# Kernel optimization log

Measured on AMD Instinct MI355X. Metric: run time of the kernel, lower is better.

The kernel has to match this reference:

```python
import jax, jax.numpy as jnp
import numpy as np

B, QS, KS = 8, 1024, 1024
QDIM = KDIM = VDIM = 512
HEADS, ODIM = 8, 64
NEG_SLOPE = 0.2


def setup_inputs() -> dict:
    key = jax.random.key(0)
    ks = jax.random.split(key, 7)
    return {
        "Q": jax.random.normal(ks[0], (B, QS, QDIM), jnp.float32),
        "K": jax.random.normal(ks[1], (B, KS, KDIM), jnp.float32),
        "V": jax.random.normal(ks[2], (B, KS, VDIM), jnp.float32),
        # torch Linear weights: (out_features, in_features)
        "WQ": jax.random.normal(ks[3], (HEADS, QDIM), jnp.float32) * 0.05,
        "WK": jax.random.normal(ks[4], (HEADS, KDIM), jnp.float32) * 0.05,
        "WV": jax.random.normal(ks[5], (HEADS * ODIM, VDIM), jnp.float32) * 0.05,
        "bias": jax.random.normal(ks[6], (HEADS, ODIM), jnp.float32) * 0.05,
    }


def reference(Q, K, V, WQ, WK, WV, bias):
    b, qs = Q.shape[:2]
    Vproj = (V @ WV.T).reshape(b, -1, HEADS, ODIM)          # (b, k, h, d)
    attn_K = K @ WK.T                                        # (b, k, h)
    attn_Q = Q @ WQ.T                                        # (b, q, h)
    # additive GAT-style scores: (b, q, k, h)
    w = jax.nn.leaky_relu(attn_Q[:, :, None, :] + attn_K[:, None, :, :],
                          negative_slope=NEG_SLOPE)
    w = jax.nn.softmax(w, axis=2)                            # softmax over keys
    out = jnp.einsum('bqkh,bkhd->bqhd', w, Vproj) + bias     # (b, q, h, d)
    return out.reshape(b, qs, -1)
```

## Files before the change

### kernel.cpp

```cpp
#include <hip/hip_runtime.h>
#include <hip/hip_bf16.h>

#define NS 0.2f


typedef _Float16 half8 __attribute__((ext_vector_type(8)));
typedef float f32x4 __attribute__((ext_vector_type(4)));

__global__ __launch_bounds__(256) void stage1_kernel(
    const float* __restrict__ Q, const float* __restrict__ K,
    const float* __restrict__ V, const float* __restrict__ WQ,
    const float* __restrict__ WK, const float* __restrict__ WV,
    float* __restrict__ aQ, float* __restrict__ aK,
    _Float16* __restrict__ Vp) {
  __shared__ __align__(16) float smem[4096];
  int bid = blockIdx.x;
  int t = threadIdx.x;
  if (bid < 4096) {
    const float* X;
    const float* W;
    float* aX;
    int rb;
    if (bid < 2048) { X = Q; W = WQ; aX = aQ; rb = bid; }
    else            { X = K; W = WK; aX = aK; rb = bid - 2048; }
    float* Wl = smem;
#pragma unroll
    for (int i = 0; i < 16; i++) Wl[i * 256 + t] = W[i * 256 + t];
    __syncthreads();
    int w = t >> 6, lane = t & 63;
    int row = rb * 4 + w;
    const float* x = X + (size_t)row * 512;
    float4 x0 = *(const float4*)(x + lane * 4);
    float4 x1 = *(const float4*)(x + 256 + lane * 4);
    float acc[8];
#pragma unroll
    for (int h = 0; h < 8; h++) {
      const float* wl = Wl + h * 512;
      float4 w0 = *(const float4*)(wl + lane * 4);
      float4 w1 = *(const float4*)(wl + 256 + lane * 4);
      float a = x0.x * w0.x + x0.y * w0.y + x0.z * w0.z + x0.w * w0.w +
                x1.x * w1.x + x1.y * w1.y + x1.z * w1.z + x1.w * w1.w;
#pragma unroll
      for (int off = 32; off > 0; off >>= 1) a += __shfl_xor(a, off);
      acc[h] = a;
    }
    if (lane == 0) {
      float* o = aX + (size_t)row * 8;
      o[0] = acc[0]; o[1] = acc[1]; o[2] = acc[2]; o[3] = acc[3];
      o[4] = acc[4]; o[5] = acc[5]; o[6] = acc[6]; o[7] = acc[7];
    }
  } else {
    int v = bid - 4096;
    int m0 = (v >> 3) * 64, n0 = (v & 7) * 64;
    _Float16* As = (_Float16*)smem;
    _Float16* Bs = (_Float16*)(smem + 1024);
    int lane = t & 63, wid = t >> 6;
    int wr = wid >> 1, wc = wid & 1;
    int sr = t >> 2, sc = t & 3;
    const float* ap = V + (size_t)(m0 + sr) * 512 + sc * 8;
    const float* bp = WV + (size_t)(n0 + sr) * 512 + sc * 8;
    _Float16* aw = As + sr * 32 + ((sc ^ ((sr >> 1) & 3)) * 8);
    _Float16* bw = Bs + sr * 32 + ((sc ^ ((sr >> 1) & 3)) * 8);
    int fr = lane & 15, fs = lane >> 4;
    f32x4 acc[2][2];
#pragma unroll
    for (int i = 0; i < 2; i++)
#pragma unroll
      for (int j = 0; j < 2; j++)
#pragma unroll
        for (int r = 0; r < 4; r++) acc[i][j][r] = 0.f;

    float4 av0 = *(const float4*)(ap);
    float4 av1 = *(const float4*)(ap + 4);
    float4 bv0 = *(const float4*)(bp);
    float4 bv1 = *(const float4*)(bp + 4);
    for (int k0 = 0; k0 < 512; k0 += 32) {
      half8 ah, bh;
      ah[0] = (_Float16)av0.x; ah[1] = (_Float16)av0.y;
      ah[2] = (_Float16)av0.z; ah[3] = (_Float16)av0.w;
      ah[4] = (_Float16)av1.x; ah[5] = (_Float16)av1.y;
      ah[6] = (_Float16)av1.z; ah[7] = (_Float16)av1.w;
      bh[0] = (_Float16)bv0.x; bh[1] = (_Float16)bv0.y;
      bh[2] = (_Float16)bv0.z; bh[3] = (_Float16)bv0.w;
      bh[4] = (_Float16)bv1.x; bh[5] = (_Float16)bv1.y;
      bh[6] = (_Float16)bv1.z; bh[7] = (_Float16)bv1.w;
      if (k0 + 32 < 512) {
        av0 = *(const float4*)(ap + k0 + 32);
        av1 = *(const float4*)(ap + k0 + 36);
        bv0 = *(const float4*)(bp + k0 + 32);
        bv1 = *(const float4*)(bp + k0 + 36);
      }
      __syncthreads();
      *(half8*)aw = ah;
      *(half8*)bw = bh;
      __syncthreads();
      half8 af[2], bf[2];
#pragma unroll
      for (int i = 0; i < 2; i++) {
        int R = wr * 32 + i * 16 + fr;
        af[i] = *(half8*)(As + R * 32 + ((fs ^ ((R >> 1) & 3)) * 8));
      }
#pragma unroll
      for (int j = 0; j < 2; j++) {
        int Cc = wc * 32 + j * 16 + fr;
        bf[j] = *(half8*)(Bs + Cc * 32 + ((fs ^ ((Cc >> 1) & 3)) * 8));
      }
#pragma unroll
      for (int i = 0; i < 2; i++)
#pragma unroll
        for (int j = 0; j < 2; j++)
          acc[i][j] = __builtin_amdgcn_mfma_f32_16x16x32_f16(
              af[i], bf[j], acc[i][j], 0, 0, 0);
    }
#pragma unroll
    for (int i = 0; i < 2; i++)
#pragma unroll
      for (int j = 0; j < 2; j++) {
        int row = m0 + wr * 32 + i * 16 + fs * 4;
        int col = n0 + wc * 32 + j * 16 + fr;
#pragma unroll
        for (int r = 0; r < 4; r++)
          Vp[(size_t)(row + r) * 512 + col] = (_Float16)acc[i][j][r];
      }
  }
}

__global__ __launch_bounds__(1024) void sortbin_kernel(
    const float* __restrict__ aK, const float* __restrict__ aQ,
    const _Float16* __restrict__ Vp, float* __restrict__ E1g,
    float* __restrict__ E2g, int* __restrict__ IDXg,
    float* __restrict__ cofs1, float* __restrict__ cofs2,
    float* __restrict__ scof1, float* __restrict__ scof2,
    float* __restrict__ amaxArr, int* __restrict__ binStart,
    int* __restrict__ binData, float* __restrict__ binX) {
  int bh = blockIdx.x, b = bh >> 3, h = bh & 7;
  __shared__ float key[1024];
  __shared__ int idx[1024];
  __shared__ float E1s[1024], E2s[1024];
  __shared__ float ct1[32][64], ct2[32][64];
  __shared__ float sct1[32], sct2[32];
  __shared__ int cnt[32], bstart[33];
  int t = threadIdx.x;
  float k = aK[(size_t)(b * 1024 + t) * 8 + h];
  int id = t;
  for (int len = 2; len <= 1024; len <<= 1) {
    bool up = ((t & len) == 0);
    for (int stride = len >> 1; stride >= 64; stride >>= 1) {
      key[t] = k; idx[t] = id;
      __syncthreads();
      int p = t ^ stride;
      float k2 = key[p];
      int i2 = idx[p];
      __syncthreads();
      bool takeMin = (((t & stride) == 0) == up);
      bool take2 = takeMin ? (k2 < k) : (k2 > k);
      if (take2) { k = k2; id = i2; }
    }
    int s0 = (len >> 1) < 32 ? (len >> 1) : 32;
    for (int stride = s0; stride >= 1; stride >>= 1) {
      float k2 = __shfl_xor(k, stride);
      int i2 = __shfl_xor(id, stride);
      bool takeMin = (((t & stride) == 0) == up);
      bool take2 = takeMin ? (k2 < k) : (k2 > k);
      if (take2) { k = k2; id = i2; }
    }
  }
  key[t] = k; idx[t] = id;
  __syncthreads();
  float amax = key[1023];
  float e1 = __expf(k - amax);
  float e2 = __expf(NS * (k - amax));
  E1s[t] = e1; E2s[t] = e2;
  E1g[bh * 1024 + t] = e1;
  E2g[bh * 1024 + t] = e2;
  IDXg[bh * 1024 + t] = id;
  if (t == 0) amaxArr[bh] = amax;
  __syncthreads();
  {
    int d = t & 63;
    const _Float16* vb = Vp + (size_t)b * 1024 * 512 + h * 64 + d;
    for (int cc = t >> 6; cc < 32; cc += 16) {
      float t1 = 0.f, t2 = 0.f;
#pragma unroll 8
      for (int j = 0; j < 32; j++) {
        int i = cc * 32 + j;
        float v = (float)vb[(size_t)idx[i] * 512];
        t1 += E1s[i] * v;
        t2 += E2s[i] * v;
      }
      ct1[cc][d] = t1; ct2[cc][d] = t2;
    }
    if (t < 32) {
      float s1 = 0.f, s2 = 0.f;
      for (int j = 0; j < 32; j++) { s1 += E1s[t * 32 + j]; s2 += E2s[t * 32 + j]; }
      sct1[t] = s1; sct2[t] = s2;
    }
  }
  __syncthreads();
  {
    int d = t & 63;
    for (int cc = t >> 6; cc < 32; cc += 16) {
      float o1 = 0.f, o2 = 0.f;
      for (int kk = cc + 1; kk < 32; kk++) o1 += ct1[kk][d];
      for (int kk = 0; kk < cc; kk++) o2 += ct2[kk][d];
      cofs1[(bh * 32 + cc) * 64 + d] = o1;
      cofs2[(bh * 32 + cc) * 64 + d] = o2;
    }
    if (t < 32) {
      float o1 = 0.f, o2 = 0.f;
      for (int kk = t + 1; kk < 32; kk++) o1 += sct1[kk];
      for (int kk = 0; kk < t; kk++) o2 += sct2[kk];
      scof1[bh * 32 + t] = o1;
      scof2[bh * 32 + t] = o2;
    }
  }
  float x = aQ[(size_t)(b * 1024 + t) * 8 + h];
  float negx = -x;
  int lo = 0, hi = 1024;
  while (lo < hi) {
    int mid = (lo + hi) >> 1;
    if (key[mid] <= negx) lo = mid + 1; else hi = mid;
  }
  int ix = lo;
  int c = ix >> 5; if (c > 31) c = 31;
  if (t < 32) cnt[t] = 0;
  __syncthreads();
  int slot = atomicAdd(&cnt[c], 1);
  __syncthreads();
  if (t == 0) {
    int s = 0;
    for (int i = 0; i < 32; i++) { bstart[i] = s; s += cnt[i]; }
    bstart[32] = s;
  }
  __syncthreads();
  if (t < 33) binStart[bh * 33 + t] = bstart[t];
  int pos = bstart[c] + slot;
  binData[bh * 1024 + pos] = (t << 11) | ix;
  binX[bh * 1024 + pos] = x;
}

__global__ __launch_bounds__(256) void final_binned(
    const float* __restrict__ E1g, const float* __restrict__ E2g,
    const int* __restrict__ IDXg, const _Float16* __restrict__ Vp,
    const float* __restrict__ cofs1, const float* __restrict__ cofs2,
    const float* __restrict__ scof1, const float* __restrict__ scof2,
    const float* __restrict__ amaxArr, const int* __restrict__ binStart,
    const int* __restrict__ binData, const float* __restrict__ binX,
    const float* __restrict__ aQ, const float* __restrict__ bias,
    float* __restrict__ out) {
  int blk = blockIdx.x;
  int bh = blk >> 5, c = blk & 31;
  int b = bh >> 3, h = bh & 7;
  int t = threadIdx.x, w = t >> 6, lane = t & 63;
  __shared__ float P1[33][64], P2[33][64];
  __shared__ float G1s[4][64], G2s[4][64];
  __shared__ float sS1[33], sS2[33];
  __shared__ float e1c[32], e2c[32];
  int n0 = binStart[bh * 33 + c];
  int n = binStart[bh * 33 + c + 1] - n0;
  if (n == 0) return;
  if (t < 32) {
    e1c[t] = E1g[bh * 1024 + c * 32 + t];
    e2c[t] = E2g[bh * 1024 + c * 32 + t];
  }
  __syncthreads();
  float f1[8], f2[8];
  {
    const _Float16* vb = Vp + (size_t)b * 1024 * 512 + h * 64 + lane;
    const int* ib = IDXg + bh * 1024 + c * 32 + w * 8;
#pragma unroll
    for (int k2 = 0; k2 < 8; k2++) {
      float v = (float)vb[(size_t)ib[k2] * 512];
      f1[k2] = e1c[w * 8 + k2] * v;
      f2[k2] = e2c[w * 8 + k2] * v;
    }
  }
  float G1 = 0.f, G2 = 0.f;
#pragma unroll
  for (int k2 = 0; k2 < 8; k2++) { G1 += f1[k2]; G2 += f2[k2]; }
  G1s[w][lane] = G1;
  G2s[w][lane] = G2;
  if (t == 0) {
    float s = 0.f;
    sS1[32] = 0.f;
    for (int l = 31; l >= 0; l--) { s += e1c[l]; sS1[l] = s; }
    s = 0.f;
    sS2[0] = 0.f;
    for (int l = 1; l <= 32; l++) { s += e2c[l - 1]; sS2[l] = s; }
  }
  __syncthreads();
  float off1 = 0.f, off2 = 0.f;
#pragma unroll
  for (int w2 = 0; w2 < 4; w2++) {
    float g1 = G1s[w2][lane], g2 = G2s[w2][lane];
    if (w2 > w) off1 += g1;
    if (w2 < w) off2 += g2;
  }
  {
    float p1v[8];
    float s = 0.f;
#pragma unroll
    for (int k2 = 7; k2 >= 0; k2--) { s += f1[k2]; p1v[k2] = s; }
#pragma unroll
    for (int k2 = 0; k2 < 8; k2++) P1[w * 8 + k2][lane] = off1 + p1v[k2];
    float p = 0.f;
#pragma unroll
    for (int k2 = 0; k2 < 8; k2++) { P2[w * 8 + k2][lane] = off2 + p; p += f2[k2]; }
    if (w == 3) P2[32][lane] = off2 + p;
    if (w == 0) P1[32][lane] = 0.f;
  }
  float o1 = cofs1[(bh * 32 + c) * 64 + lane];
  float o2 = cofs2[(bh * 32 + c) * 64 + lane];
  float so1 = scof1[bh * 32 + c];
  float so2 = scof2[bh * 32 + c];
  float amax = amaxArr[bh];
  float bi = bias[h * 64 + lane];
  __syncthreads();
  for (int qi = w; qi < n; qi += 4) {
    int rec = binData[bh * 1024 + n0 + qi];
    float x = binX[bh * 1024 + n0 + qi];
    int q = rec >> 11;
    int l = (rec & 2047) - c * 32;
    float num1 = o1 + P1[l][lane];
    float num2 = o2 + P2[l][lane];
    float xs = x + amax;
    float ex = __expf(xs), e2x = __expf(NS * xs);
    float Z = ex * (so1 + sS1[l]) + e2x * (so2 + sS2[l]);
    out[((size_t)(b * 1024 + q)) * 512 + h * 64 + lane] =
        (ex * num1 + e2x * num2) / Z + bi;
  }
}

__global__ __launch_bounds__(256) void projQK_kernel(
    const float* __restrict__ Q, const float* __restrict__ K,
    const float* __restrict__ WQ, const float* __restrict__ WK,
    float* __restrict__ aQ, float* __restrict__ aK) {
  int bid = blockIdx.x;
  const float* X;
  const float* W;
  float* aX;
  int rb;
  if (bid < 2048) { X = Q; W = WQ; aX = aQ; rb = bid; }
  else            { X = K; W = WK; aX = aK; rb = bid - 2048; }
  __shared__ __align__(16) float Wl[8 * 512];
  int t = threadIdx.x;
#pragma unroll
  for (int i = 0; i < 16; i++) Wl[i * 256 + t] = W[i * 256 + t];
  __syncthreads();
  int w = t >> 6, lane = t & 63;
  int row = rb * 4 + w;
  const float* x = X + (size_t)row * 512;
  float4 x0 = *(const float4*)(x + lane * 4);
  float4 x1 = *(const float4*)(x + 256 + lane * 4);
  float acc[8];
#pragma unroll
  for (int h = 0; h < 8; h++) {
    const float* wl = Wl + h * 512;
    float4 w0 = *(const float4*)(wl + lane * 4);
    float4 w1 = *(const float4*)(wl + 256 + lane * 4);
    float a = x0.x * w0.x + x0.y * w0.y + x0.z * w0.z + x0.w * w0.w +
              x1.x * w1.x + x1.y * w1.y + x1.z * w1.z + x1.w * w1.w;
#pragma unroll
    for (int off = 32; off > 0; off >>= 1) a += __shfl_xor(a, off);
    acc[h] = a;
  }
  if (lane == 0) {
    float* o = aX + (size_t)row * 8;
    o[0] = acc[0]; o[1] = acc[1]; o[2] = acc[2]; o[3] = acc[3];
    o[4] = acc[4]; o[5] = acc[5]; o[6] = acc[6]; o[7] = acc[7];
  }
}

__global__ __launch_bounds__(256) void vproj_gemm(
    const float* __restrict__ A, const float* __restrict__ Wv,
    float* __restrict__ C) {
  __shared__ __align__(16) float As[16][68];
  __shared__ __align__(16) float Bs[16][68];
  int t = threadIdx.x;
  int m0 = blockIdx.x * 64, n0 = blockIdx.y * 64;
  int tx = t & 15, ty = t >> 4;
  int lr = t >> 2, lk = (t & 3) * 4;
  float acc[4][4] = {{0.f}};
  const float* ap = A + (size_t)(m0 + lr) * 512 + lk;
  const float* bp = Wv + (size_t)(n0 + lr) * 512 + lk;
  for (int k0 = 0; k0 < 512; k0 += 16) {
    float4 av = *(const float4*)(ap + k0);
    float4 bv = *(const float4*)(bp + k0);
    __syncthreads();
    As[lk + 0][lr] = av.x; As[lk + 1][lr] = av.y;
    As[lk + 2][lr] = av.z; As[lk + 3][lr] = av.w;
    Bs[lk + 0][lr] = bv.x; Bs[lk + 1][lr] = bv.y;
    Bs[lk + 2][lr] = bv.z; Bs[lk + 3][lr] = bv.w;
    __syncthreads();
#pragma unroll
    for (int kk = 0; kk < 16; kk++) {
      float4 a4 = *(const float4*)&As[kk][ty * 4];
      float4 b4 = *(const float4*)&Bs[kk][tx * 4];
      float aa[4] = {a4.x, a4.y, a4.z, a4.w};
      float bb[4] = {b4.x, b4.y, b4.z, b4.w};
#pragma unroll
      for (int i = 0; i < 4; i++)
#pragma unroll
        for (int j = 0; j < 4; j++) acc[i][j] += aa[i] * bb[j];
    }
  }
#pragma unroll
  for (int i = 0; i < 4; i++) {
    float4 o = {acc[i][0], acc[i][1], acc[i][2], acc[i][3]};
    *(float4*)(C + (size_t)(m0 + ty * 4 + i) * 512 + n0 + tx * 4) = o;
  }
}

__global__ __launch_bounds__(256) void direct_kernel(
    const float* __restrict__ aQ, const float* __restrict__ aK,
    const float* __restrict__ Vp, const float* __restrict__ bias,
    float* __restrict__ out) {
  int id = blockIdx.x;
  int qt = id & 15, h = (id >> 4) & 7, b = id >> 7;
  __shared__ float AK[1024], E1s[1024], E2s[1024];
  __shared__ __align__(16) float VT[128][64];
  __shared__ float XQ[64];
  int t = threadIdx.x;
  for (int i = t; i < 1024; i += 256) {
    float a = aK[(size_t)(b * 1024 + i) * 8 + h];
    AK[i] = a; E1s[i] = __expf(a); E2s[i] = __expf(NS * a);
  }
  if (t < 64) XQ[t] = aQ[(size_t)(b * 1024 + qt * 64 + t) * 8 + h];
  __syncthreads();
  int w = t >> 6, d = t & 63;
  float xq[16], ex[16], e2x[16], acc[16], z[16];
#pragma unroll
  for (int qi = 0; qi < 16; qi++) {
    float x = XQ[w * 16 + qi];
    xq[qi] = x; ex[qi] = __expf(x); e2x[qi] = __expf(NS * x);
    acc[qi] = 0.f; z[qi] = 0.f;
  }
  for (int kt = 0; kt < 8; kt++) {
    __syncthreads();
    for (int i = t; i < 128 * 64; i += 256) {
      VT[i >> 6][i & 63] =
          Vp[(size_t)(b * 1024 + kt * 128 + (i >> 6)) * 512 + h * 64 + (i & 63)];
    }
    __syncthreads();
    for (int kk = 0; kk < 128; kk++) {
      int k = kt * 128 + kk;
      float a = AK[k], e1 = E1s[k], e2 = E2s[k];
      float v = VT[kk][d];
#pragma unroll
      for (int qi = 0; qi < 16; qi++) {
        float wsel = (a + xq[qi] > 0.f) ? (ex[qi] * e1) : (e2x[qi] * e2);
        acc[qi] += wsel * v;
        z[qi] += wsel;
      }
    }
  }
#pragma unroll
  for (int qi = 0; qi < 16; qi++) {
    int q = qt * 64 + w * 16 + qi;
    out[(size_t)(b * 1024 + q) * 512 + h * 64 + d] =
        acc[qi] / z[qi] + bias[h * 64 + d];
  }
}

extern "C" void kernel_launch(void* const* d_in, const int* in_sizes, int n_in,
                              void* d_out, int out_size, void* d_ws,
                              size_t ws_size, hipStream_t stream) {
  const float* Q = (const float*)d_in[0];
  const float* K = (const float*)d_in[1];
  const float* V = (const float*)d_in[2];
  const float* WQ = (const float*)d_in[3];
  const float* WK = (const float*)d_in[4];
  const float* WV = (const float*)d_in[5];
  const float* bias = (const float*)d_in[6];
  float* out = (float*)d_out;
  char* ws = (char*)d_ws;

  const size_t oAQ   = 0;
  const size_t oAK   = 262144;
  const size_t oE1   = 524288;
  const size_t oE2   = 786432;
  const size_t oIDX  = 1048576;
  const size_t oCOF1 = 1310720;
  const size_t oCOF2 = 1835008;
  const size_t oSC1  = 2359296;
  const size_t oSC2  = 2375680;
  const size_t oAMX  = 2392064;
  const size_t oBST  = 2396160;
  const size_t oBDA  = 2412544;
  const size_t oBX   = 2674688;
  const size_t oVP   = 2936832;
  const size_t NEED_MAIN = oVP + 8388608;
  const size_t NEED_FB = 524288 + 16777216;

  if (ws_size >= NEED_MAIN) {
    float* aQ = (float*)(ws + oAQ);
    float* aK = (float*)(ws + oAK);
    float* E1g = (float*)(ws + oE1);
    float* E2g = (float*)(ws + oE2);
    int* IDXg = (int*)(ws + oIDX);
    float* cofs1 = (float*)(ws + oCOF1);
    float* cofs2 = (float*)(ws + oCOF2);
    float* scof1 = (float*)(ws + oSC1);
    float* scof2 = (float*)(ws + oSC2);
    float* amaxA = (float*)(ws + oAMX);
    int* binSt = (int*)(ws + oBST);
    int* binDa = (int*)(ws + oBDA);
    float* binX = (float*)(ws + oBX);
    _Float16* Vp = (_Float16*)(ws + oVP);
    hipLaunchKernelGGL(stage1_kernel, dim3(5120), dim3(256), 0, stream, Q, K,
                       V, WQ, WK, WV, aQ, aK, Vp);
    hipLaunchKernelGGL(sortbin_kernel, dim3(64), dim3(1024), 0, stream, aK, aQ,
                       Vp, E1g, E2g, IDXg, cofs1, cofs2, scof1, scof2, amaxA,
                       binSt, binDa, binX);
    hipLaunchKernelGGL(final_binned, dim3(2048), dim3(256), 0, stream, E1g,
                       E2g, IDXg, Vp, cofs1, cofs2, scof1, scof2, amaxA, binSt,
                       binDa, binX, aQ, bias, out);
  } else if (ws_size >= NEED_FB) {
    float* aQ = (float*)(ws + 0);
    float* aK = (float*)(ws + 262144);
    float* Vpf = (float*)(ws + 524288);
    hipLaunchKernelGGL(projQK_kernel, dim3(4096), dim3(256), 0, stream, Q, K,
                       WQ, WK, aQ, aK);
    hipLaunchKernelGGL(vproj_gemm, dim3(128, 8), dim3(256), 0, stream, V, WV,
                       Vpf);
    hipLaunchKernelGGL(direct_kernel, dim3(1024), dim3(256), 0, stream, aQ, aK,
                       Vpf, bias, out);
  }
}
```

Before: 73.65 us.

## Split fused stage1 into QK projection and deeper-K MFMA V-projection kernels

Replaces the single fused stage1 kernel with two launches. The first is a QK projection kernel where each block handles 16 rows instead of 4, so the shared-memory weight load is amortized over four times as many rows. The second is a dedicated fp16 MFMA GEMM for the V projection that uses a 64-wide K step, halving the number of barrier pairs per tile. This gives up the single-launch overlap of the two kinds of work and adds an extra kernel launch, in exchange for better weight reuse and fewer synchronizations.

```diff
diff --git a/kernel.cpp b/kernel.cpp
--- a/kernel.cpp
+++ b/kernel.cpp
@@ -7,28 +7,26 @@
 typedef _Float16 half8 __attribute__((ext_vector_type(8)));
 typedef float f32x4 __attribute__((ext_vector_type(4)));
 
-__global__ __launch_bounds__(256) void stage1_kernel(
+__global__ __launch_bounds__(256) void projQK_kernel(
     const float* __restrict__ Q, const float* __restrict__ K,
-    const float* __restrict__ V, const float* __restrict__ WQ,
-    const float* __restrict__ WK, const float* __restrict__ WV,
-    float* __restrict__ aQ, float* __restrict__ aK,
-    _Float16* __restrict__ Vp) {
-  __shared__ __align__(16) float smem[4096];
+    const float* __restrict__ WQ, const float* __restrict__ WK,
+    float* __restrict__ aQ, float* __restrict__ aK) {
   int bid = blockIdx.x;
+  const float* X;
+  const float* W;
+  float* aX;
+  int rb;
+  if (bid < 512) { X = Q; W = WQ; aX = aQ; rb = bid; }
+  else           { X = K; W = WK; aX = aK; rb = bid - 512; }
+  __shared__ __align__(16) float Wl[8 * 512];
   int t = threadIdx.x;
-  if (bid < 4096) {
-    const float* X;
-    const float* W;
-    float* aX;
-    int rb;
-    if (bid < 2048) { X = Q; W = WQ; aX = aQ; rb = bid; }
-    else            { X = K; W = WK; aX = aK; rb = bid - 2048; }
-    float* Wl = smem;
-#pragma unroll
-    for (int i = 0; i < 16; i++) Wl[i * 256 + t] = W[i * 256 + t];
-    __syncthreads();
-    int w = t >> 6, lane = t & 63;
-    int row = rb * 4 + w;
+#pragma unroll
+  for (int i = 0; i < 16; i++) Wl[i * 256 + t] = W[i * 256 + t];
+  __syncthreads();
+  int w = t >> 6, lane = t & 63;
+#pragma unroll
+  for (int r = 0; r < 4; r++) {
+    int row = rb * 16 + w * 4 + r;
     const float* x = X + (size_t)row * 512;
     float4 x0 = *(const float4*)(x + lane * 4);
     float4 x1 = *(const float4*)(x + 256 + lane * 4);
@@ -49,80 +47,112 @@
       o[0] = acc[0]; o[1] = acc[1]; o[2] = acc[2]; o[3] = acc[3];
       o[4] = acc[4]; o[5] = acc[5]; o[6] = acc[6]; o[7] = acc[7];
     }
-  } else {
-    int v = bid - 4096;
-    int m0 = (v >> 3) * 64, n0 = (v & 7) * 64;
-    _Float16* As = (_Float16*)smem;
-    _Float16* Bs = (_Float16*)(smem + 1024);
-    int lane = t & 63, wid = t >> 6;
-    int wr = wid >> 1, wc = wid & 1;
-    int sr = t >> 2, sc = t & 3;
-    const float* ap = V + (size_t)(m0 + sr) * 512 + sc * 8;
-    const float* bp = WV + (size_t)(n0 + sr) * 512 + sc * 8;
-    _Float16* aw = As + sr * 32 + ((sc ^ ((sr >> 1) & 3)) * 8);
-    _Float16* bw = Bs + sr * 32 + ((sc ^ ((sr >> 1) & 3)) * 8);
-    int fr = lane & 15, fs = lane >> 4;
-    f32x4 acc[2][2];
+  }
+}
+
+__global__ __launch_bounds__(256) void vproj_mfma(
+    const float* __restrict__ A, const float* __restrict__ Wv,
+    _Float16* __restrict__ C) {
+  __shared__ __align__(16) _Float16 As[64 * 64];
+  __shared__ __align__(16) _Float16 Bs[64 * 64];
+  int t = threadIdx.x;
+  int m0 = blockIdx.x * 64, n0 = blockIdx.y * 64;
+  int lane = t & 63, wid = t >> 6;
+  int wr = wid >> 1, wc = wid & 1;
+  int sr = t >> 2, sc = t & 3;
+  const float* ap = A + (size_t)(m0 + sr) * 512 + sc * 16;
+  const float* bp = Wv + (size_t)(n0 + sr) * 512 + sc * 16;
+  int swz = sr & 7;
+  _Float16* aw0 = As + sr * 64 + (((2 * sc + 0) ^ swz) * 8);
+  _Float16* aw1 = As + sr * 64 + (((2 * sc + 1) ^ swz) * 8);
+  _Float16* bw0 = Bs + sr * 64 + (((2 * sc + 0) ^ swz) * 8);
+  _Float16* bw1 = Bs + sr * 64 + (((2 * sc + 1) ^ swz) * 8);
+  int fr = lane & 15, fs = lane >> 4;
+  f32x4 acc[2][2];
+#pragma unroll
+  for (int i = 0; i < 2; i++)
+#pragma unroll
+    for (int j = 0; j < 2; j++)
+#pragma unroll
+      for (int r = 0; r < 4; r++) acc[i][j][r] = 0.f;
+
+  float4 a0 = *(const float4*)(ap);
+  float4 a1 = *(const float4*)(ap + 4);
+  float4 a2 = *(const float4*)(ap + 8);
+  float4 a3 = *(const float4*)(ap + 12);
+  float4 b0 = *(const float4*)(bp);
+  float4 b1 = *(const float4*)(bp + 4);
+  float4 b2 = *(const float4*)(bp + 8);
+  float4 b3 = *(const float4*)(bp + 12);
+  for (int k0 = 0; k0 < 512; k0 += 64) {
+    half8 ah0, ah1, bh0, bh1;
+    ah0[0] = (_Float16)a0.x; ah0[1] = (_Float16)a0.y;
+    ah0[2] = (_Float16)a0.z; ah0[3] = (_Float16)a0.w;
+    ah0[4] = (_Float16)a1.x; ah0[5] = (_Float16)a1.y;
+    ah0[6] = (_Float16)a1.z; ah0[7] = (_Float16)a1.w;
+    ah1[0] = (_Float16)a2.x; ah1[1] = (_Float16)a2.y;
+    ah1[2] = (_Float16)a2.z; ah1[3] = (_Float16)a2.w;
+    ah1[4] = (_Float16)a3.x; ah1[5] = (_Float16)a3.y;
+    ah1[6] = (_Float16)a3.z; ah1[7] = (_Float16)a3.w;
+    bh0[0] = (_Float16)b0.x; bh0[1] = (_Float16)b0.y;
+    bh0[2] = (_Float16)b0.z; bh0[3] = (_Float16)b0.w;
+    bh0[4] = (_Float16)b1.x; bh0[5] = (_Float16)b1.y;
+    bh0[6] = (_Float16)b1.z; bh0[7] = (_Float16)b1.w;
+    bh1[0] = (_Float16)b2.x; bh1[1] = (_Float16)b2.y;
+    bh1[2] = (_Float16)b2.z; bh1[3] = (_Float16)b2.w;
+    bh1[4] = (_Float16)b3.x; bh1[5] = (_Float16)b3.y;
+    bh1[6] = (_Float16)b3.z; bh1[7] = (_Float16)b3.w;
+    if (k0 + 64 < 512) {
+      a0 = *(const float4*)(ap + k0 + 64);
+      a1 = *(const float4*)(ap + k0 + 68);
+      a2 = *(const float4*)(ap + k0 + 72);
+      a3 = *(const float4*)(ap + k0 + 76);
+      b0 = *(const float4*)(bp + k0 + 64);
+      b1 = *(const float4*)(bp + k0 + 68);
+      b2 = *(const float4*)(bp + k0 + 72);
+      b3 = *(const float4*)(bp + k0 + 76);
+    }
+    __syncthreads();
+    *(half8*)aw0 = ah0;
+    *(half8*)aw1 = ah1;
+    *(half8*)bw0 = bh0;
+    *(half8*)bw1 = bh1;
+    __syncthreads();
+    half8 af[2][2], bf[2][2];
+#pragma unroll
+    for (int i = 0; i < 2; i++) {
+      int R = wr * 32 + i * 16 + fr;
+#pragma unroll
+      for (int kk = 0; kk < 2; kk++)
+        af[i][kk] = *(half8*)(As + R * 64 + (((fs + 4 * kk) ^ (R & 7)) * 8));
+    }
+#pragma unroll
+    for (int j = 0; j < 2; j++) {
+      int Cc = wc * 32 + j * 16 + fr;
+#pragma unroll
+      for (int kk = 0; kk < 2; kk++)
+        bf[j][kk] = *(half8*)(Bs + Cc * 64 + (((fs + 4 * kk) ^ (Cc & 7)) * 8));
+    }
 #pragma unroll
     for (int i = 0; i < 2; i++)
 #pragma unroll
-      for (int j = 0; j < 2; j++)
-#pragma unroll
-        for (int r = 0; r < 4; r++) acc[i][j][r] = 0.f;
-
-    float4 av0 = *(const float4*)(ap);
-    float4 av1 = *(const float4*)(ap + 4);
-    float4 bv0 = *(const float4*)(bp);
-    float4 bv1 = *(const float4*)(bp + 4);
-    for (int k0 = 0; k0 < 512; k0 += 32) {
-      half8 ah, bh;
-      ah[0] = (_Float16)av0.x; ah[1] = (_Float16)av0.y;
-      ah[2] = (_Float16)av0.z; ah[3] = (_Float16)av0.w;
-      ah[4] = (_Float16)av1.x; ah[5] = (_Float16)av1.y;
-      ah[6] = (_Float16)av1.z; ah[7] = (_Float16)av1.w;
-      bh[0] = (_Float16)bv0.x; bh[1] = (_Float16)bv0.y;
-      bh[2] = (_Float16)bv0.z; bh[3] = (_Float16)bv0.w;
-      bh[4] = (_Float16)bv1.x; bh[5] = (_Float16)bv1.y;
-      bh[6] = (_Float16)bv1.z; bh[7] = (_Float16)bv1.w;
-      if (k0 + 32 < 512) {
-        av0 = *(const float4*)(ap + k0 + 32);
-        av1 = *(const float4*)(ap + k0 + 36);
-        bv0 = *(const float4*)(bp + k0 + 32);
-        bv1 = *(const float4*)(bp + k0 + 36);
+      for (int j = 0; j < 2; j++) {
+        acc[i][j] = __builtin_amdgcn_mfma_f32_16x16x32_f16(
+            af[i][0], bf[j][0], acc[i][j], 0, 0, 0);
+        acc[i][j] = __builtin_amdgcn_mfma_f32_16x16x32_f16(
+            af[i][1], bf[j][1], acc[i][j], 0, 0, 0);
       }
-      __syncthreads();
-      *(half8*)aw = ah;
-      *(half8*)bw = bh;
-      __syncthreads();
-      half8 af[2], bf[2];
-#pragma unroll
-      for (int i = 0; i < 2; i++) {
-        int R = wr * 32 + i * 16 + fr;
-        af[i] = *(half8*)(As + R * 32 + ((fs ^ ((R >> 1) & 3)) * 8));
-      }
-#pragma unroll
-      for (int j = 0; j < 2; j++) {
-        int Cc = wc * 32 + j * 16 + fr;
-        bf[j] = *(half8*)(Bs + Cc * 32 + ((fs ^ ((Cc >> 1) & 3)) * 8));
-      }
-#pragma unroll
-      for (int i = 0; i < 2; i++)
-#pragma unroll
-        for (int j = 0; j < 2; j++)
-          acc[i][j] = __builtin_amdgcn_mfma_f32_16x16x32_f16(
-              af[i], bf[j], acc[i][j], 0, 0, 0);
-    }
-#pragma unroll
-    for (int i = 0; i < 2; i++)
-#pragma unroll
-      for (int j = 0; j < 2; j++) {
-        int row = m0 + wr * 32 + i * 16 + fs * 4;
-        int col = n0 + wc * 32 + j * 16 + fr;
-#pragma unroll
-        for (int r = 0; r < 4; r++)
-          Vp[(size_t)(row + r) * 512 + col] = (_Float16)acc[i][j][r];
-      }
-  }
+  }
+#pragma unroll
+  for (int i = 0; i < 2; i++)
+#pragma unroll
+    for (int j = 0; j < 2; j++) {
+      int row = m0 + wr * 32 + i * 16 + fs * 4;
+      int col = n0 + wc * 32 + j * 16 + fr;
+#pragma unroll
+      for (int r = 0; r < 4; r++)
+        C[(size_t)(row + r) * 512 + col] = (_Float16)acc[i][j][r];
+    }
 }
 
 __global__ __launch_bounds__(1024) void sortbin_kernel(
@@ -331,46 +361,6 @@
   }
 }
 
-__global__ __launch_bounds__(256) void projQK_kernel(
-    const float* __restrict__ Q, const float* __restrict__ K,
-    const float* __restrict__ WQ, const float* __restrict__ WK,
-    float* __restrict__ aQ, float* __restrict__ aK) {
-  int bid = blockIdx.x;
-  const float* X;
-  const float* W;
-  float* aX;
-  int rb;
-  if (bid < 2048) { X = Q; W = WQ; aX = aQ; rb = bid; }
-  else            { X = K; W = WK; aX = aK; rb = bid - 2048; }
-  __shared__ __align__(16) float Wl[8 * 512];
-  int t = threadIdx.x;
-#pragma unroll
-  for (int i = 0; i < 16; i++) Wl[i * 256 + t] = W[i * 256 + t];
-  __syncthreads();
-  int w = t >> 6, lane = t & 63;
-  int row = rb * 4 + w;
-  const float* x = X + (size_t)row * 512;
-  float4 x0 = *(const float4*)(x + lane * 4);
-  float4 x1 = *(const float4*)(x + 256 + lane * 4);
-  float acc[8];
-#pragma unroll
-  for (int h = 0; h < 8; h++) {
-    const float* wl = Wl + h * 512;
-    float4 w0 = *(const float4*)(wl + lane * 4);
-    float4 w1 = *(const float4*)(wl + 256 + lane * 4);
-    float a = x0.x * w0.x + x0.y * w0.y + x0.z * w0.z + x0.w * w0.w +
-              x1.x * w1.x + x1.y * w1.y + x1.z * w1.z + x1.w * w1.w;
-#pragma unroll
-    for (int off = 32; off > 0; off >>= 1) a += __shfl_xor(a, off);
-    acc[h] = a;
-  }
-  if (lane == 0) {
-    float* o = aX + (size_t)row * 8;
-    o[0] = acc[0]; o[1] = acc[1]; o[2] = acc[2]; o[3] = acc[3];
-    o[4] = acc[4]; o[5] = acc[5]; o[6] = acc[6]; o[7] = acc[7];
-  }
-}
-
 __global__ __launch_bounds__(256) void vproj_gemm(
     const float* __restrict__ A, const float* __restrict__ Wv,
     float* __restrict__ C) {
@@ -462,6 +452,49 @@
   }
 }
 
+__global__ __launch_bounds__(256) void projQK_fb_kernel(
+    const float* __restrict__ Q, const float* __restrict__ K,
+    const float* __restrict__ WQ, const float* __restrict__ WK,
+    float* __restrict__ aQ, float* __restrict__ aK) {
+  int bid = blockIdx.x;
+  const float* X;
+  const float* W;
+  float* aX;
+  int rb;
+  if (bid < 512) { X = Q; W = WQ; aX = aQ; rb = bid; }
+  else           { X = K; W = WK; aX = aK; rb = bid - 512; }
+  __shared__ __align__(16) float Wl[8 * 512];
+  int t = threadIdx.x;
+#pragma unroll
+  for (int i = 0; i < 16; i++) Wl[i * 256 + t] = W[i * 256 + t];
+  __syncthreads();
+  int w = t >> 6, lane = t & 63;
+#pragma unroll
+  for (int r = 0; r < 4; r++) {
+    int row = rb * 16 + w * 4 + r;
+    const float* x = X + (size_t)row * 512;
+    float4 x0 = *(const float4*)(x + lane * 4);
+    float4 x1 = *(const float4*)(x + 256 + lane * 4);
+    float acc[8];
+#pragma unroll
+    for (int h = 0; h < 8; h++) {
+      const float* wl = Wl + h * 512;
+      float4 w0 = *(const float4*)(wl + lane * 4);
+      float4 w1 = *(const float4*)(wl + 256 + lane * 4);
+      float a = x0.x * w0.x + x0.y * w0.y + x0.z * w0.z + x0.w * w0.w +
+                x1.x * w1.x + x1.y * w1.y + x1.z * w1.z + x1.w * w1.w;
+#pragma unroll
+      for (int off = 32; off > 0; off >>= 1) a += __shfl_xor(a, off);
+      acc[h] = a;
+    }
+    if (lane == 0) {
+      float* o = aX + (size_t)row * 8;
+      o[0] = acc[0]; o[1] = acc[1]; o[2] = acc[2]; o[3] = acc[3];
+      o[4] = acc[4]; o[5] = acc[5]; o[6] = acc[6]; o[7] = acc[7];
+    }
+  }
+}
+
 extern "C" void kernel_launch(void* const* d_in, const int* in_sizes, int n_in,
                               void* d_out, int out_size, void* d_ws,
                               size_t ws_size, hipStream_t stream) {
@@ -507,8 +540,10 @@
     int* binDa = (int*)(ws + oBDA);
     float* binX = (float*)(ws + oBX);
     _Float16* Vp = (_Float16*)(ws + oVP);
-    hipLaunchKernelGGL(stage1_kernel, dim3(5120), dim3(256), 0, stream, Q, K,
-                       V, WQ, WK, WV, aQ, aK, Vp);
+    hipLaunchKernelGGL(projQK_kernel, dim3(1024), dim3(256), 0, stream, Q, K,
+                       WQ, WK, aQ, aK);
+    hipLaunchKernelGGL(vproj_mfma, dim3(128, 8), dim3(256), 0, stream, V, WV,
+                       Vp);
     hipLaunchKernelGGL(sortbin_kernel, dim3(64), dim3(1024), 0, stream, aK, aQ,
                        Vp, E1g, E2g, IDXg, cofs1, cofs2, scof1, scof2, amaxA,
                        binSt, binDa, binX);
@@ -519,8 +554,8 @@
     float* aQ = (float*)(ws + 0);
     float* aK = (float*)(ws + 262144);
     float* Vpf = (float*)(ws + 524288);
-    hipLaunchKernelGGL(projQK_kernel, dim3(4096), dim3(256), 0, stream, Q, K,
-                       WQ, WK, aQ, aK);
+    hipLaunchKernelGGL(projQK_fb_kernel, dim3(1024), dim3(256), 0, stream, Q,
+                       K, WQ, WK, aQ, aK);
     hipLaunchKernelGGL(vproj_gemm, dim3(128, 8), dim3(256), 0, stream, V, WV,
                        Vpf);
     hipLaunchKernelGGL(direct_kernel, dim3(1024), dim3(256), 0, stream, aQ, aK,
```

Measured after the change: 72.42 us. About the same (-1.7%).
